# Kernel optimization log

Hardware: AMD Instinct MI355X
Metric: run time of the kernel (lower is better)

Reference implementation:

```python
import jax, jax.numpy as jnp
import numpy as np

EPS = 1e-08

def _compute_W(V, C, eps=EPS):
    # W = H_k ... H_1, applied sequentially as in the torch loop
    W = jnp.eye(C, dtype=V.dtype)
    def step(W, v):
        v = v / (jnp.linalg.norm(v) + eps)
        # H @ W = W - 2 v (v^T W)
        W = W - 2.0 * jnp.outer(v, v @ W)
        return W, None
    W, _ = jax.lax.scan(step, W, V)
    return W

def setup_inputs() -> dict:
    key = jax.random.key(0)
    k1, k2 = jax.random.split(key)
    x = jax.random.normal(k1, (16, 512, 64, 64), dtype=jnp.float32)
    V = jax.random.normal(k2, (32, 512), dtype=jnp.float32)
    return {"x": x, "V": V}

def reference(x, V):
    B, C, H, Wd = x.shape
    W = _compute_W(V, C)  # [C, C] orthogonal
    # 1x1 conv: out[b,o,h,w] = sum_c W[o,c] * x[b,c,h,w]
    return jnp.einsum('oc,bchw->bohw', W, x)
```

## Files before the change

kernel.cpp:

```cpp
#include <hip/hip_runtime.h>
#include <hip/hip_bf16.h>
#include <stdint.h>
#include <stddef.h>

#define HH_EPS 1e-8f

typedef __attribute__((ext_vector_type(8))) short short8;
typedef __attribute__((ext_vector_type(4))) float f32x4;

#define CDIM 512
#define SDIM 4096
#define BN 64
#define BK 32
#define NSTEP 16
#define BROW 40

__device__ __forceinline__ size_t wt_idx(int o, int c) {
    return ((size_t)((c >> 5) * 32 + (o >> 4)) * 64
            + (size_t)((o & 15) * 4 + ((c >> 3) & 3))) * 8 + (c & 7);
}

__global__ void compute_w(const float* __restrict__ V,
                          __hip_bfloat16* __restrict__ Wt) {
    const int wave = threadIdx.x >> 6;
    const int lane = threadIdx.x & 63;
    const int jA = (blockIdx.x * 4 + wave) * 2;
    const int jB = jA + 1;
    const int ib = lane * 8;

    float wA[8], wB[8];
    #pragma unroll
    for (int r = 0; r < 8; r++) {
        wA[r] = (ib + r == jA) ? 1.0f : 0.0f;
        wB[r] = (ib + r == jB) ? 1.0f : 0.0f;
    }
    float4 c0 = *(const float4*)(V + ib);
    float4 c1 = *(const float4*)(V + ib + 4);

    for (int k = 0; k < 32; k++) {
        const float v[8] = {c0.x, c0.y, c0.z, c0.w, c1.x, c1.y, c1.z, c1.w};
        if (k < 31) {
            c0 = *(const float4*)(V + (size_t)(k + 1) * 512 + ib);
            c1 = *(const float4*)(V + (size_t)(k + 1) * 512 + ib + 4);
        }
        float dA = 0.0f, dB = 0.0f, ss = 0.0f;
        #pragma unroll
        for (int r = 0; r < 8; r++) {
            dA += v[r] * wA[r];
            dB += v[r] * wB[r];
            ss += v[r] * v[r];
        }
        #pragma unroll
        for (int off = 32; off > 0; off >>= 1) {
            dA += __shfl_xor(dA, off);
            dB += __shfl_xor(dB, off);
            ss += __shfl_xor(ss, off);
        }
        const float t = sqrtf(ss) + HH_EPS;
        const float scale = 2.0f / (t * t);
        const float tA = scale * dA, tB = scale * dB;
        #pragma unroll
        for (int r = 0; r < 8; r++) {
            wA[r] -= tA * v[r];
            wB[r] -= tB * v[r];
        }
    }
    #pragma unroll
    for (int r = 0; r < 8; r++) {
        Wt[wt_idx(ib + r, jA)] = __float2bfloat16(wA[r]);
        Wt[wt_idx(ib + r, jB)] = __float2bfloat16(wB[r]);
    }
}

__device__ __forceinline__ void gld_lds16(const void* g, void* l) {
    __builtin_amdgcn_global_load_lds(
        (const __attribute__((address_space(1))) uint32_t*)g,
        (__attribute__((address_space(3))) uint32_t*)l, 16, 0, 0);
}

template<int N> __device__ __forceinline__ void wait_vm() {
    __builtin_amdgcn_s_waitcnt((N & 15) | ((N >> 4) << 14) | (7 << 4) | (15 << 8));
}

__device__ __forceinline__ void lds_barrier() {
    __builtin_amdgcn_s_waitcnt(0xC07F);
    __builtin_amdgcn_s_barrier();
}

constexpr int vm_after_A(int kt) {
    int n = 0;
    if (kt + 1 < NSTEP) n += 8;
    if (kt + 2 < NSTEP) n += 8;
    if (kt + 3 < NSTEP) n += 8;
    return n;
}

__global__ __launch_bounds__(256, 2) void hh_gemm(
    const float* __restrict__ x,
    const __hip_bfloat16* __restrict__ Wt,
    float* __restrict__ out)
{
    __shared__ __attribute__((aligned(16))) __hip_bfloat16 Albuf[2][512 * BK];
    __shared__ __attribute__((aligned(16))) __hip_bfloat16 Bbuf[2][BN * BROW];

    const int tid  = threadIdx.x;
    const int wave = tid >> 6, lane = tid & 63;
    const int quad = lane >> 4, l16 = lane & 15;

    const int bid = blockIdx.x;
    const int b   = bid >> 6;
    const int nt  = bid & 63;
    const int n0  = nt * BN;

    const float* xb = x + (size_t)b * CDIM * SDIM;
    const int bn = tid & 63;
    const float* xp0 = xb + (size_t)(wave * 8) * SDIM + n0 + bn;

    f32x4 acc[8][4];
    #pragma unroll
    for (int mi = 0; mi < 8; mi++)
        #pragma unroll
        for (int ni = 0; ni < 4; ni++) {
            f32x4 z = {0.0f, 0.0f, 0.0f, 0.0f};
            acc[mi][ni] = z;
        }

    float pfB[3][8];

    auto loadA = [&](int kt, int p) {
        const char* gbase = (const char*)Wt
            + ((size_t)kt * 32 + (size_t)wave * 8) * 1024 + (size_t)lane * 16;
        char* lbase = (char*)&Albuf[p][(size_t)(wave * 8) * 512];
        #pragma unroll
        for (int i = 0; i < 8; i++)
            gld_lds16(gbase + (size_t)i * 1024, lbase + (size_t)i * 1024);
    };
    auto loadB = [&](int kt, float* dst) {
        const float* p = xp0 + (size_t)kt * BK * SDIM;
        #pragma unroll
        for (int j = 0; j < 8; j++) dst[j] = p[(size_t)j * SDIM];
    };
    auto writeB = [&](int buf, const float* src) {
        short8 pk;
        #pragma unroll
        for (int j = 0; j < 8; j++) {
            __hip_bfloat16 h = __float2bfloat16(src[j]);
            pk[j] = *(short*)&h;
        }
        *(short8*)(&Bbuf[buf][bn * BROW + wave * 8]) = pk;
    };

    loadA(0, 0);
    loadB(0, pfB[0]);
    loadB(1, pfB[1]);
    loadB(2, pfB[2]);
    writeB(0, pfB[0]);
    lds_barrier();

#define DO_STEP(KT)                                                            \
    {                                                                          \
        constexpr int p = (KT) & 1;                                            \
        if constexpr ((KT) + 1 < NSTEP) loadA((KT) + 1, p ^ 1);                \
        if constexpr ((KT) + 3 < NSTEP) loadB((KT) + 3, pfB[(KT) % 3]);        \
        wait_vm<vm_after_A(KT)>();    \
        short8 afr[8], bfr[4];                                                 \
        _Pragma("unroll")                                                      \
        for (int mi = 0; mi < 8; mi++)                                         \
            afr[mi] = *(const short8*)(&Albuf[p][(wave * 8 + mi) * 512         \
                                                 + (l16 * 4 + quad) * 8]);     \
        _Pragma("unroll")                                                      \
        for (int ni = 0; ni < 4; ni++)                                         \
            bfr[ni] = *(const short8*)(&Bbuf[p][(ni * 16 + l16) * BROW         \
                                                + quad * 8]);                  \
        _Pragma("unroll")                                                      \
        for (int mi = 0; mi < 8; mi++)                                         \
            _Pragma("unroll")                                                  \
            for (int ni = 0; ni < 4; ni++)                                     \
                acc[mi][ni] = __builtin_amdgcn_mfma_f32_16x16x32_bf16(         \
                    afr[mi], bfr[ni], acc[mi][ni], 0, 0, 0);                   \
        if constexpr ((KT) + 1 < NSTEP) {                                      \
            writeB(p ^ 1, pfB[((KT) + 1) % 3]);                                \
            lds_barrier();                                                     \
        }                                                                      \
    }

    DO_STEP(0)  DO_STEP(1)  DO_STEP(2)  DO_STEP(3)
    DO_STEP(4)  DO_STEP(5)  DO_STEP(6)  DO_STEP(7)
    DO_STEP(8)  DO_STEP(9)  DO_STEP(10) DO_STEP(11)
    DO_STEP(12) DO_STEP(13) DO_STEP(14) DO_STEP(15)
#undef DO_STEP

    float* ob = out + (size_t)b * CDIM * SDIM + n0;
    #pragma unroll
    for (int mi = 0; mi < 8; mi++) {
        #pragma unroll
        for (int ni = 0; ni < 4; ni++) {
            const int col = ni * 16 + l16;
            #pragma unroll
            for (int r = 0; r < 4; r++) {
                const int row = wave * 128 + mi * 16 + quad * 4 + r;
                ob[(size_t)row * SDIM + col] = acc[mi][ni][r];
            }
        }
    }
}

extern "C" void kernel_launch(void* const* d_in, const int* in_sizes, int n_in,
                              void* d_out, int out_size, void* d_ws, size_t ws_size,
                              hipStream_t stream) {
    const float* x = (const float*)d_in[0];
    const float* V = (const float*)d_in[1];
    float* out = (float*)d_out;

    __hip_bfloat16* Wt = (__hip_bfloat16*)d_ws;

    compute_w<<<64, 256, 0, stream>>>(V, Wt);
    hh_gemm<<<1024, 256, 0, stream>>>(x, Wt, out);
}
```

Before: 272.4 us.

## Widen GEMM tile to 128 columns with 512 threads and swapped MFMA operands

Doubles the spatial tile per block and the block to 512 threads (8 waves as 4 output groups by 2 column halves), re-lays out Wt and the B tile so MFMA fragments are read contiguously per lane, and swaps operand roles so each lane's accumulator holds 4 consecutive spatial outputs. That allows vectorized 16-byte nontemporal output stores instead of scalar strided stores. It also deepens the x prefetch to 4 stages, uses nontemporal loads, and moves the vmem wait to just before the barrier. The aim is to halve the per-output reload of W and improve store coalescing, in exchange for more registers per thread and fewer blocks in the grid.

```diff
diff --git a/kernel.cpp b/kernel.cpp
--- a/kernel.cpp
+++ b/kernel.cpp
@@ -10,14 +10,13 @@
 
 #define CDIM 512
 #define SDIM 4096
-#define BN 64
+#define BN 128
 #define BK 32
 #define NSTEP 16
-#define BROW 40
 
 __device__ __forceinline__ size_t wt_idx(int o, int c) {
-    return ((size_t)((c >> 5) * 32 + (o >> 4)) * 64
-            + (size_t)((o & 15) * 4 + ((c >> 3) & 3))) * 8 + (c & 7);
+    return ((((size_t)(c >> 5) * 4 + (o >> 7)) * 8 + ((o >> 4) & 7)) * 64
+            + (size_t)((c >> 3) & 3) * 16 + (o & 15)) * 8 + (c & 7);
 }
 
 __global__ void compute_w(const float* __restrict__ V,
@@ -87,58 +86,55 @@
     __builtin_amdgcn_s_barrier();
 }
 
-constexpr int vm_after_A(int kt) {
-    int n = 0;
-    if (kt + 1 < NSTEP) n += 8;
-    if (kt + 2 < NSTEP) n += 8;
-    if (kt + 3 < NSTEP) n += 8;
-    return n;
-}
-
-__global__ __launch_bounds__(256, 2) void hh_gemm(
+constexpr int vm_pre(int kt) { return (kt + 4 < NSTEP) ? 8 : 0; }
+
+__global__ __launch_bounds__(512, 2) void hh_gemm(
     const float* __restrict__ x,
     const __hip_bfloat16* __restrict__ Wt,
     float* __restrict__ out)
 {
-    __shared__ __attribute__((aligned(16))) __hip_bfloat16 Albuf[2][512 * BK];
-    __shared__ __attribute__((aligned(16))) __hip_bfloat16 Bbuf[2][BN * BROW];
+    __shared__ __attribute__((aligned(16))) __hip_bfloat16 Albuf[2][CDIM * BK];
+    __shared__ __attribute__((aligned(16))) __hip_bfloat16 Bbuf[2][BN * BK];
 
     const int tid  = threadIdx.x;
     const int wave = tid >> 6, lane = tid & 63;
+    const int ow = wave & 3, nh = wave >> 2;
     const int quad = lane >> 4, l16 = lane & 15;
 
     const int bid = blockIdx.x;
-    const int b   = bid >> 6;
-    const int nt  = bid & 63;
+    const int b   = bid >> 5;
+    const int nt  = bid & 31;
     const int n0  = nt * BN;
 
     const float* xb = x + (size_t)b * CDIM * SDIM;
-    const int bn = tid & 63;
-    const float* xp0 = xb + (size_t)(wave * 8) * SDIM + n0 + bn;
-
-    f32x4 acc[8][4];
-    #pragma unroll
-    for (int mi = 0; mi < 8; mi++)
-        #pragma unroll
-        for (int ni = 0; ni < 4; ni++) {
+    const int bn = tid & 127;
+    const int kq = tid >> 7;
+    const float* xp0 = xb + (size_t)(kq * 8) * SDIM + n0 + bn;
+
+    f32x4 acc[4][8];
+    #pragma unroll
+    for (int mi = 0; mi < 4; mi++)
+        #pragma unroll
+        for (int oi = 0; oi < 8; oi++) {
             f32x4 z = {0.0f, 0.0f, 0.0f, 0.0f};
-            acc[mi][ni] = z;
-        }
-
-    float pfB[3][8];
+            acc[mi][oi] = z;
+        }
+
+    float pfB[4][8];
 
     auto loadA = [&](int kt, int p) {
         const char* gbase = (const char*)Wt
-            + ((size_t)kt * 32 + (size_t)wave * 8) * 1024 + (size_t)lane * 16;
-        char* lbase = (char*)&Albuf[p][(size_t)(wave * 8) * 512];
-        #pragma unroll
-        for (int i = 0; i < 8; i++)
+            + ((size_t)(kt * 4 + ow) * 8 + nh * 4) * 1024 + (size_t)lane * 16;
+        char* lbase = (char*)&Albuf[p][0] + (size_t)(ow * 8 + nh * 4) * 1024;
+        #pragma unroll
+        for (int i = 0; i < 4; i++)
             gld_lds16(gbase + (size_t)i * 1024, lbase + (size_t)i * 1024);
     };
     auto loadB = [&](int kt, float* dst) {
         const float* p = xp0 + (size_t)kt * BK * SDIM;
         #pragma unroll
-        for (int j = 0; j < 8; j++) dst[j] = p[(size_t)j * SDIM];
+        for (int j = 0; j < 8; j++)
+            dst[j] = __builtin_nontemporal_load(p + (size_t)j * SDIM);
     };
     auto writeB = [&](int buf, const float* src) {
         short8 pk;
@@ -147,40 +143,42 @@
             __hip_bfloat16 h = __float2bfloat16(src[j]);
             pk[j] = *(short*)&h;
         }
-        *(short8*)(&Bbuf[buf][bn * BROW + wave * 8]) = pk;
+        *(short8*)(&Bbuf[buf][(size_t)(((bn >> 4) * 4 + kq) * 16 + (bn & 15)) * 8]) = pk;
     };
 
     loadA(0, 0);
     loadB(0, pfB[0]);
     loadB(1, pfB[1]);
     loadB(2, pfB[2]);
+    loadB(3, pfB[3]);
     writeB(0, pfB[0]);
+    wait_vm<24>();
     lds_barrier();
 
 #define DO_STEP(KT)                                                            \
     {                                                                          \
         constexpr int p = (KT) & 1;                                            \
         if constexpr ((KT) + 1 < NSTEP) loadA((KT) + 1, p ^ 1);                \
-        if constexpr ((KT) + 3 < NSTEP) loadB((KT) + 3, pfB[(KT) % 3]);        \
-        wait_vm<vm_after_A(KT)>();    \
-        short8 afr[8], bfr[4];                                                 \
+        if constexpr ((KT) + 4 < NSTEP) loadB((KT) + 4, pfB[(KT) % 4]);        \
+        short8 afr[4], bfr[8];                                                 \
         _Pragma("unroll")                                                      \
-        for (int mi = 0; mi < 8; mi++)                                         \
-            afr[mi] = *(const short8*)(&Albuf[p][(wave * 8 + mi) * 512         \
-                                                 + (l16 * 4 + quad) * 8]);     \
+        for (int mi = 0; mi < 4; mi++)                                         \
+            afr[mi] = *(const short8*)(&Bbuf[p][(size_t)((nh * 4 + mi) * 64    \
+                                                         + lane) * 8]);       \
         _Pragma("unroll")                                                      \
-        for (int ni = 0; ni < 4; ni++)                                         \
-            bfr[ni] = *(const short8*)(&Bbuf[p][(ni * 16 + l16) * BROW         \
-                                                + quad * 8]);                  \
+        for (int oi = 0; oi < 8; oi++)                                         \
+            bfr[oi] = *(const short8*)(&Albuf[p][(size_t)((ow * 8 + oi) * 64   \
+                                                          + lane) * 8]);      \
         _Pragma("unroll")                                                      \
-        for (int mi = 0; mi < 8; mi++)                                         \
+        for (int mi = 0; mi < 4; mi++)                                         \
             _Pragma("unroll")                                                  \
-            for (int ni = 0; ni < 4; ni++)                                     \
-                acc[mi][ni] = __builtin_amdgcn_mfma_f32_16x16x32_bf16(         \
-                    afr[mi], bfr[ni], acc[mi][ni], 0, 0, 0);                   \
+            for (int oi = 0; oi < 8; oi++)                                     \
+                acc[mi][oi] = __builtin_amdgcn_mfma_f32_16x16x32_bf16(         \
+                    afr[mi], bfr[oi], acc[mi][oi], 0, 0, 0);                   \
         if constexpr ((KT) + 1 < NSTEP) {                                      \
-            writeB(p ^ 1, pfB[((KT) + 1) % 3]);                                \
-            lds_barrier();                                                     \
+            writeB(p ^ 1, pfB[((KT) + 1) % 4]);                                \
+            wait_vm<vm_pre(KT)>();    \
+            lds_barrier();                    \
         }                                                                      \
     }
 
@@ -190,17 +188,14 @@
     DO_STEP(12) DO_STEP(13) DO_STEP(14) DO_STEP(15)
 #undef DO_STEP
 
-    float* ob = out + (size_t)b * CDIM * SDIM + n0;
-    #pragma unroll
-    for (int mi = 0; mi < 8; mi++) {
-        #pragma unroll
-        for (int ni = 0; ni < 4; ni++) {
-            const int col = ni * 16 + l16;
-            #pragma unroll
-            for (int r = 0; r < 4; r++) {
-                const int row = wave * 128 + mi * 16 + quad * 4 + r;
-                ob[(size_t)row * SDIM + col] = acc[mi][ni][r];
-            }
+    float* ob = out + (size_t)b * CDIM * SDIM + n0 + nh * 64;
+    #pragma unroll
+    for (int oi = 0; oi < 8; oi++) {
+        const int o = ow * 128 + oi * 16 + l16;
+        #pragma unroll
+        for (int mi = 0; mi < 4; mi++) {
+            f32x4* dst = (f32x4*)(ob + (size_t)o * SDIM + mi * 16 + quad * 4);
+            __builtin_nontemporal_store(acc[mi][oi], dst);
         }
     }
 }
@@ -215,5 +210,5 @@
     __hip_bfloat16* Wt = (__hip_bfloat16*)d_ws;
 
     compute_w<<<64, 256, 0, stream>>>(V, Wt);
-    hh_gemm<<<1024, 256, 0, stream>>>(x, Wt, out);
-}
+    hh_gemm<<<512, 512, 0, stream>>>(x, Wt, out);
+}
```

Result: no change. 275.2 us (+1.0%).
